# Kernel tuning notes

Measured on AMD Instinct MI355X. Metric: run time of the kernel, lower is better.

The kernel has to match this reference:

```python
import jax, jax.numpy as jnp
import numpy as np

N, FIN, FOUT = 4096, 256, 256


def setup_inputs() -> dict:
    key = jax.random.key(0)
    ks = jax.random.split(key, 6)
    x = jax.random.normal(ks[0], (N, FIN), jnp.float32)
    adj = jax.random.randint(ks[1], (N, N), 0, 2, jnp.int32)  # dense 0/1 adjacency
    W = jax.random.normal(ks[2], (FOUT, FIN), jnp.float32) / np.sqrt(FIN)
    b = jax.random.normal(ks[3], (FOUT,), jnp.float32) * 0.01
    att_w = jax.random.normal(ks[4], (2 * FOUT,), jnp.float32) / np.sqrt(2.0 * FOUT)  # Linear(2F,1).weight squeezed
    att_b = jax.random.normal(ks[5], (), jnp.float32) * 0.01
    return {"x": x, "adj": adj, "W": W, "b": b, "att_w": att_w, "att_b": att_b}


def reference(x, adj, W, b, att_w, att_b):
    n = x.shape[0]
    fo = W.shape[0]
    h = x @ W.T + b  # [N, Fout]
    # score(i,j) = att([h_i ; h_j]) = h_i.w1 + h_j.w2 + att_b  -> no [N,N,2F] concat
    s = (h @ att_w[:fo])[:, None] + (h @ att_w[fo:])[None, :] + att_b  # [N, N]
    edge = adj == 1
    # GLOBAL softmax over all edges (faithful to F.softmax(stacked_scores, dim=0))
    gmax = jnp.max(jnp.where(edge, s, -jnp.inf))
    e = jnp.exp(s - gmax)
    denom = jnp.sum(jnp.where(edge, e, 0.0))
    p = (e / denom).reshape(-1)  # softmaxed score per pair (valid at edges)
    # original indexes attention_scores[j] by NODE id j into the row-major edge list:
    # recover the score of the j-th global edge (j = 0..N-1) via cumsum rank + scatter
    flat = edge.reshape(-1)
    rank = jnp.cumsum(flat.astype(jnp.int32)) - 1  # rank of each edge in row-major order
    idx = jnp.where(flat, rank, n)  # non-edges and ranks >= n get dropped
    w_node = jnp.zeros((n,), h.dtype).at[idx].set(p, mode="drop")  # [N]
    # output[i] = sum_{j: adj[i,j]==1} w_node[j] * h[j]
    out = jax.nn.relu(edge.astype(h.dtype) @ (w_node[:, None] * h))
    return out
```

## Files before the change

kernel.cpp:

```cpp
#include <hip/hip_runtime.h>
#include <cstdint>
#include <cstddef>

#define NN 4096
#define FDIM 256

typedef __attribute__((ext_vector_type(4))) float fx4;
typedef __attribute__((ext_vector_type(2))) float fx2;
typedef __attribute__((ext_vector_type(8))) short s8v;

__device__ inline uint16_t f2bf(float f) {
    union { float f; uint32_t u; } v; v.f = f;
    uint32_t u = v.u;
    uint32_t r = (u + 0x7FFFu + ((u >> 16) & 1u)) >> 16;
    return (uint16_t)r;
}

__global__ __launch_bounds__(256) void k_h(const float* __restrict__ x,
        const float* __restrict__ W, const float* __restrict__ bias,
        float* __restrict__ h) {
    __shared__ __align__(16) float xs[2][64 * 34];
    __shared__ __align__(16) float wt[2][64 * 68];
    const int bi = blockIdx.x, bf = blockIdx.y;
    const int t = threadIdx.x;
    const int tx = t & 15, ty = t >> 4;
    float acc[2][4] = {};
    float rx[8], rw[16];
    #pragma unroll
    for (int u = 0; u < 8; ++u) {
        const int e = t + 256 * u, r = e >> 6, c = e & 63;
        rx[u] = x[(size_t)(bi * 32 + r) * 256 + c];
    }
    #pragma unroll
    for (int u = 0; u < 16; ++u) {
        const int e = t + 256 * u, r = e >> 6, c = e & 63;
        rw[u] = W[(size_t)(bf * 64 + r) * 256 + c];
    }
    for (int p = 0; p < 4; ++p) {
        float* xb = xs[p & 1];
        float* wb = wt[p & 1];
        #pragma unroll
        for (int u = 0; u < 8; ++u) {
            const int e = t + 256 * u, r = e >> 6, c = e & 63;
            xb[c * 34 + r] = rx[u];
        }
        #pragma unroll
        for (int u = 0; u < 16; ++u) {
            const int e = t + 256 * u, r = e >> 6, c = e & 63;
            const int sw = 8 * ((c & 7) ^ ((c >> 3) & 7));
            wb[c * 68 + (r ^ sw)] = rw[u];
        }
        __syncthreads();
        if (p < 3) {
            const int k0 = (p + 1) * 64;
            #pragma unroll
            for (int u = 0; u < 8; ++u) {
                const int e = t + 256 * u, r = e >> 6, c = e & 63;
                rx[u] = x[(size_t)(bi * 32 + r) * 256 + k0 + c];
            }
            #pragma unroll
            for (int u = 0; u < 16; ++u) {
                const int e = t + 256 * u, r = e >> 6, c = e & 63;
                rw[u] = W[(size_t)(bf * 64 + r) * 256 + k0 + c];
            }
        }
        #pragma unroll 16
        for (int k = 0; k < 64; ++k) {
            const int sw = 8 * ((k & 7) ^ ((k >> 3) & 7));
            const fx2 av = *(const fx2*)(xb + k * 34 + ty * 2);
            const fx4 bv = *(const fx4*)(wb + k * 68 + ((tx * 4) ^ sw));
            #pragma unroll
            for (int u = 0; u < 2; ++u)
                #pragma unroll
                for (int v = 0; v < 4; ++v)
                    acc[u][v] += av[u] * bv[v];
        }
    }
    const fx4 bv = *(const fx4*)(bias + bf * 64 + tx * 4);
    #pragma unroll
    for (int u = 0; u < 2; ++u) {
        const int i = bi * 32 + ty * 2 + u;
        fx4 r;
        #pragma unroll
        for (int v = 0; v < 4; ++v) r[v] = acc[u][v] + bv[v];
        *(fx4*)(h + (size_t)i * 256 + bf * 64 + tx * 4) = r;
    }
}

__global__ __launch_bounds__(256) void k_a(const float* __restrict__ h,
        const float* __restrict__ att_w, float* __restrict__ a1,
        float* __restrict__ a2) {
    const int wv = threadIdx.x >> 6, l = threadIdx.x & 63;
    const int i = blockIdx.x * 4 + wv;
    float s1 = 0.f, s2 = 0.f;
    #pragma unroll
    for (int c = l; c < 256; c += 64) {
        const float hv = h[(size_t)i * 256 + c];
        s1 += hv * att_w[c];
        s2 += hv * att_w[256 + c];
    }
    #pragma unroll
    for (int d = 32; d > 0; d >>= 1) {
        s1 += __shfl_down(s1, d);
        s2 += __shfl_down(s2, d);
    }
    if (l == 0) { a1[i] = s1; a2[i] = s2; }
}

__global__ __launch_bounds__(1024) void k_prep(const float* __restrict__ a1,
        const float* __restrict__ a2, const int* __restrict__ adj,
        float* __restrict__ E1, float* __restrict__ E2,
        float* __restrict__ wraw, float* __restrict__ Sg) {
    __shared__ float E1s[NN];
    __shared__ float E2s[NN];
    __shared__ float red1[16], red2[16];
    __shared__ int wtot[16];
    __shared__ int base_s;
    const int t = threadIdx.x, lane = t & 63, wv = t >> 6;
    const fx4 v1 = *(const fx4*)(a1 + t * 4);
    const fx4 v2 = *(const fx4*)(a2 + t * 4);
    float m1 = fmaxf(fmaxf(v1[0], v1[1]), fmaxf(v1[2], v1[3]));
    float m2 = fmaxf(fmaxf(v2[0], v2[1]), fmaxf(v2[2], v2[3]));
    #pragma unroll
    for (int d = 32; d > 0; d >>= 1) {
        m1 = fmaxf(m1, __shfl_down(m1, d));
        m2 = fmaxf(m2, __shfl_down(m2, d));
    }
    if (lane == 0) { red1[wv] = m1; red2[wv] = m2; }
    __syncthreads();
    if (t == 0) {
        float mm1 = -1e30f, mm2 = -1e30f;
        for (int k = 0; k < 16; ++k) {
            mm1 = fmaxf(mm1, red1[k]);
            mm2 = fmaxf(mm2, red2[k]);
        }
        red1[0] = mm1; red2[0] = mm2;
        *Sg = 0.f;
        base_s = 0;
    }
    __syncthreads();
    const float M1 = red1[0], M2 = red2[0];
    fx4 e1v, e2v, z4 = {0.f, 0.f, 0.f, 0.f};
    #pragma unroll
    for (int j = 0; j < 4; ++j) {
        e1v[j] = expf(v1[j] - M1);
        e2v[j] = expf(v2[j] - M2);
    }
    *(fx4*)(E1s + t * 4) = e1v;
    *(fx4*)(E2s + t * 4) = e2v;
    *(fx4*)(E1 + t * 4) = e1v;
    *(fx4*)(E2 + t * 4) = e2v;
    *(fx4*)(wraw + t * 4) = z4;
    __syncthreads();
    for (int row = 0; row < NN; ++row) {
        const int base = base_s;
        if (base >= NN) break;
        const int4 a = ((const int4*)(adj + (size_t)row * NN))[t];
        const int vj[4] = {a.x, a.y, a.z, a.w};
        int cnt = 0;
        #pragma unroll
        for (int j = 0; j < 4; ++j) cnt += (vj[j] == 1);
        int inc = cnt;
        #pragma unroll
        for (int d = 1; d < 64; d <<= 1) {
            const int y = __shfl_up(inc, d);
            if (lane >= d) inc += y;
        }
        if (lane == 63) wtot[wv] = inc;
        __syncthreads();
        int wbase = 0, total = 0;
        #pragma unroll
        for (int w = 0; w < 16; ++w) {
            const int xw = wtot[w];
            total += xw;
            wbase += (w < wv) ? xw : 0;
        }
        if (t == 0) base_s = base + total;
        int r = base + wbase + inc - cnt;
        if (cnt && r < NN) {
            const float e1 = E1s[row];
            #pragma unroll
            for (int j = 0; j < 4; ++j) {
                if (vj[j] == 1) {
                    if (r < NN) wraw[r] = e1 * E2s[t * 4 + j];
                    ++r;
                }
            }
        }
        __syncthreads();
    }
}

__global__ __launch_bounds__(256) void k_g(const float* __restrict__ h,
        const float* __restrict__ wraw, uint16_t* __restrict__ gt) {
    __shared__ float tile[64][65];
    const int bj = blockIdx.x, bf = blockIdx.y;
    const int t = threadIdx.x;
    for (int e = t; e < 4096; e += 256) {
        const int r = e >> 6, c = e & 63;
        const int j = bj * 64 + r;
        tile[r][c] = h[(size_t)j * 256 + bf * 64 + c] * wraw[j];
    }
    __syncthreads();
    for (int e = t; e < 4096; e += 256) {
        const int r = e >> 6, c = e & 63;
        gt[(size_t)(bf * 64 + r) * NN + bj * 64 + c] = f2bf(tile[c][r]);
    }
}

__global__ __launch_bounds__(256) void k_fused(const int* __restrict__ adj,
        const uint16_t* __restrict__ gt, const float* __restrict__ E1,
        const float* __restrict__ E2, float* __restrict__ part,
        float* __restrict__ Sg, int krange) {
    __shared__ __align__(16) uint16_t As[64 * 72];
    __shared__ __align__(16) uint16_t Gs[272 * 72];
    const int ib = blockIdx.x, ks = blockIdx.y;
    const int t = threadIdx.x;
    const int wv = t >> 6, lane = t & 63;
    const int q = lane >> 4, m16 = lane & 15;
    const int i0 = ib * 64, k0 = ks * krange;
    const int ksteps = krange >> 6;

    fx4 acc[4][4];
    #pragma unroll
    for (int a = 0; a < 4; ++a)
        #pragma unroll
        for (int b = 0; b < 4; ++b) acc[a][b] = (fx4){0.f, 0.f, 0.f, 0.f};
    fx4 accS[4];
    #pragma unroll
    for (int a = 0; a < 4; ++a) accS[a] = (fx4){0.f, 0.f, 0.f, 0.f};

    for (int e = t; e < 15 * 72; e += 256) Gs[257 * 72 + e] = 0;

    for (int step = 0; step < ksteps; ++step) {
        const int kk = k0 + step * 64;
        #pragma unroll
        for (int p = 0; p < 4; ++p) {
            const int r = p * 16 + (t >> 4);
            const int c4 = (t & 15) * 4;
            const int4 a = *(const int4*)(adj + (size_t)(i0 + r) * NN + kk + c4);
            uint2 w;
            w.x = (uint32_t)(a.x | (a.y << 16)) * 0x3F80u;
            w.y = (uint32_t)(a.z | (a.w << 16)) * 0x3F80u;
            *(uint2*)(&As[r * 72 + c4]) = w;
        }
        #pragma unroll
        for (int p = 0; p < 8; ++p) {
            const int f = p * 32 + (t >> 3);
            const int ch = (t & 7) * 8;
            const s8v v = *(const s8v*)(gt + (size_t)f * NN + kk + ch);
            *(s8v*)(Gs + f * 72 + ch) = v;
        }
        if (t < 8) {
            const float* e2p = E2 + kk + t * 8;
            uint32_t* dst = (uint32_t*)(&Gs[256 * 72 + t * 8]);
            #pragma unroll
            for (int j = 0; j < 4; ++j)
                dst[j] = (uint32_t)f2bf(e2p[2 * j]) |
                         ((uint32_t)f2bf(e2p[2 * j + 1]) << 16);
        }
        __syncthreads();
        s8v afr[4][2];
        #pragma unroll
        for (int it = 0; it < 4; ++it)
            #pragma unroll
            for (int kh = 0; kh < 2; ++kh)
                afr[it][kh] = *(const s8v*)(As + (it * 16 + m16) * 72 + kh * 32 + q * 8);
        #pragma unroll
        for (int ft = 0; ft < 4; ++ft) {
            #pragma unroll
            for (int kh = 0; kh < 2; ++kh) {
                const s8v bfr = *(const s8v*)(Gs + (wv * 64 + ft * 16 + m16) * 72 + kh * 32 + q * 8);
                #pragma unroll
                for (int it = 0; it < 4; ++it)
                    acc[it][ft] = __builtin_amdgcn_mfma_f32_16x16x32_bf16(
                        afr[it][kh], bfr, acc[it][ft], 0, 0, 0);
            }
        }
        if (wv == 3) {
            #pragma unroll
            for (int kh = 0; kh < 2; ++kh) {
                const s8v bfrS = *(const s8v*)(Gs + (256 + m16) * 72 + kh * 32 + q * 8);
                #pragma unroll
                for (int it = 0; it < 4; ++it)
                    accS[it] = __builtin_amdgcn_mfma_f32_16x16x32_bf16(
                        afr[it][kh], bfrS, accS[it], 0, 0, 0);
            }
        }
        __syncthreads();
    }
    if (wv == 3) {
        float s_local = 0.f;
        #pragma unroll
        for (int it = 0; it < 4; ++it)
            #pragma unroll
            for (int r = 0; r < 4; ++r)
                s_local += accS[it][r] * E1[i0 + it * 16 + q * 4 + r];
        #pragma unroll
        for (int d = 32; d > 0; d >>= 1) s_local += __shfl_down(s_local, d);
        if (lane == 0) atomicAdd(Sg, s_local);
    }
    float* dst = part + (size_t)ks * NN * FDIM;
    #pragma unroll
    for (int it = 0; it < 4; ++it) {
        #pragma unroll
        for (int ft = 0; ft < 4; ++ft) {
            const int f = wv * 64 + ft * 16 + m16;
            #pragma unroll
            for (int r = 0; r < 4; ++r) {
                const int i = i0 + it * 16 + q * 4 + r;
                dst[(size_t)i * FDIM + f] = acc[it][ft][r];
            }
        }
    }
}

__global__ __launch_bounds__(256) void k_out(const float* __restrict__ part,
        const float* __restrict__ Sg, float* __restrict__ out, int nsplit) {
    const int b = blockIdx.x;
    const int ib = (b & 7) + 8 * ((b >> 3) & 7);
    const int sub = b >> 6;
    const int t = threadIdx.x;
    const int row = ib * 64 + sub * 4 + (t >> 6);
    const size_t idx = (size_t)row * 256 + (t & 63) * 4;
    const float inv = 1.0f / (*Sg);
    fx4 s = {0.f, 0.f, 0.f, 0.f};
    for (int k = 0; k < nsplit; ++k)
        s += *(const fx4*)(part + (size_t)k * NN * FDIM + idx);
    fx4 r;
    r[0] = fmaxf(s[0], 0.f) * inv;
    r[1] = fmaxf(s[1], 0.f) * inv;
    r[2] = fmaxf(s[2], 0.f) * inv;
    r[3] = fmaxf(s[3], 0.f) * inv;
    *(fx4*)(out + idx) = r;
}

extern "C" void kernel_launch(void* const* d_in, const int* in_sizes, int n_in,
                              void* d_out, int out_size, void* d_ws, size_t ws_size,
                              hipStream_t stream) {
    const float* x     = (const float*)d_in[0];
    const int*   adj   = (const int*)d_in[1];
    const float* W     = (const float*)d_in[2];
    const float* bias  = (const float*)d_in[3];
    const float* att_w = (const float*)d_in[4];
    float* out = (float*)d_out;
    char* ws = (char*)d_ws;
    float*    h    = (float*)(ws + 0);
    uint16_t* gt   = (uint16_t*)(ws + (size_t)4194304);
    float*    a1   = (float*)(ws + 6291456);
    float*    a2   = (float*)(ws + 6307840);
    float*    E1   = (float*)(ws + 6324224);
    float*    E2   = (float*)(ws + 6340608);
    float*    wraw = (float*)(ws + 6356992);
    float*    Sg   = (float*)(ws + 6373376);
    float*    part = (float*)(ws + 6373632);

    const size_t avail = (ws_size > 6373632) ? (ws_size - 6373632) : 0;
    int splitk = 1;
    while (splitk < 8 &&
           (size_t)(splitk * 2) * NN * FDIM * sizeof(float) <= avail)
        splitk <<= 1;
    const int krange = NN / splitk;

    k_h   <<<dim3(128, 4), 256, 0, stream>>>(x, W, bias, h);
    k_a   <<<dim3(1024), 256, 0, stream>>>(h, att_w, a1, a2);
    k_prep<<<dim3(1), 1024, 0, stream>>>(a1, a2, adj, E1, E2, wraw, Sg);
    k_g   <<<dim3(64, 4), 256, 0, stream>>>(h, wraw, gt);
    k_fused<<<dim3(64, splitk), 256, 0, stream>>>(adj, gt, E1, E2, part, Sg, krange);
    k_out <<<dim3(1024), 256, 0, stream>>>(part, Sg, out, splitk);
}
```

Before: 159.5 us.

## Fuse all stages into one cooperative persistent kernel with grid syncs

Replaces the six separate kernel launches with a single cooperative kernel of 512 blocks that runs every stage, separated by grid-wide barriers, to remove launch gaps and inter-kernel drain. It falls back to the old multi-kernel path if the cooperative launch fails or the workspace is too small. The prep stage now runs on a single 256-thread block instead of 1024 threads, so its serial row scan is slower and leaves the rest of the grid idle at the barrier. The k_out indexing is also simplified.

```diff
diff --git a/kernel.cpp b/kernel.cpp
--- a/kernel.cpp
+++ b/kernel.cpp
@@ -1,6 +1,9 @@
 #include <hip/hip_runtime.h>
+#include <hip/hip_cooperative_groups.h>
 #include <cstdint>
 #include <cstddef>
+
+namespace cg = cooperative_groups;
 
 #define NN 4096
 #define FDIM 256
@@ -14,6 +17,340 @@
     uint32_t u = v.u;
     uint32_t r = (u + 0x7FFFu + ((u >> 16) & 1u)) >> 16;
     return (uint16_t)r;
+}
+
+union SMem {
+    struct { float xs[2 * 64 * 34]; float wt[2 * 64 * 68]; } p1;
+    struct { float E1s[NN]; float E2s[NN]; float red1[4], red2[4];
+             int wtot[4]; int base_s; } p3;
+    struct { float tile[32 * 65]; } p4;
+    struct { uint16_t As[64 * 72]; uint16_t Gs[272 * 72]; } p5;
+};
+
+__global__ __launch_bounds__(256, 2) void k_mega(
+        const float* __restrict__ x, const int* __restrict__ adj,
+        const float* __restrict__ W, const float* __restrict__ bias,
+        const float* __restrict__ att_w,
+        float* __restrict__ h, uint16_t* __restrict__ gt,
+        float* __restrict__ a1, float* __restrict__ a2,
+        float* __restrict__ E1, float* __restrict__ E2,
+        float* __restrict__ wraw, float* __restrict__ Sg,
+        float* __restrict__ part, float* __restrict__ out) {
+    cg::grid_group grid = cg::this_grid();
+    __shared__ SMem sm;
+    const int blk = blockIdx.x;
+    const int t = threadIdx.x;
+    const int lane = t & 63, wv = t >> 6;
+
+    {
+        const int bi = blk & 127, bf = blk >> 7;
+        const int tx = t & 15, ty = t >> 4;
+        float acc[2][4] = {};
+        float rx[8], rw[16];
+        #pragma unroll
+        for (int u = 0; u < 8; ++u) {
+            const int e = t + 256 * u, r = e >> 6, c = e & 63;
+            rx[u] = x[(size_t)(bi * 32 + r) * 256 + c];
+        }
+        #pragma unroll
+        for (int u = 0; u < 16; ++u) {
+            const int e = t + 256 * u, r = e >> 6, c = e & 63;
+            rw[u] = W[(size_t)(bf * 64 + r) * 256 + c];
+        }
+        for (int p = 0; p < 4; ++p) {
+            float* xb = sm.p1.xs + (p & 1) * (64 * 34);
+            float* wb = sm.p1.wt + (p & 1) * (64 * 68);
+            #pragma unroll
+            for (int u = 0; u < 8; ++u) {
+                const int e = t + 256 * u, r = e >> 6, c = e & 63;
+                xb[c * 34 + r] = rx[u];
+            }
+            #pragma unroll
+            for (int u = 0; u < 16; ++u) {
+                const int e = t + 256 * u, r = e >> 6, c = e & 63;
+                const int sw = 8 * ((c & 7) ^ ((c >> 3) & 7));
+                wb[c * 68 + (r ^ sw)] = rw[u];
+            }
+            __syncthreads();
+            if (p < 3) {
+                const int k0 = (p + 1) * 64;
+                #pragma unroll
+                for (int u = 0; u < 8; ++u) {
+                    const int e = t + 256 * u, r = e >> 6, c = e & 63;
+                    rx[u] = x[(size_t)(bi * 32 + r) * 256 + k0 + c];
+                }
+                #pragma unroll
+                for (int u = 0; u < 16; ++u) {
+                    const int e = t + 256 * u, r = e >> 6, c = e & 63;
+                    rw[u] = W[(size_t)(bf * 64 + r) * 256 + k0 + c];
+                }
+            }
+            #pragma unroll 16
+            for (int k = 0; k < 64; ++k) {
+                const int sw = 8 * ((k & 7) ^ ((k >> 3) & 7));
+                const fx2 av = *(const fx2*)(xb + k * 34 + ty * 2);
+                const fx4 bv = *(const fx4*)(wb + k * 68 + ((tx * 4) ^ sw));
+                #pragma unroll
+                for (int u = 0; u < 2; ++u)
+                    #pragma unroll
+                    for (int v = 0; v < 4; ++v)
+                        acc[u][v] += av[u] * bv[v];
+            }
+        }
+        const fx4 bv = *(const fx4*)(bias + bf * 64 + tx * 4);
+        #pragma unroll
+        for (int u = 0; u < 2; ++u) {
+            const int i = bi * 32 + ty * 2 + u;
+            fx4 r;
+            #pragma unroll
+            for (int v = 0; v < 4; ++v) r[v] = acc[u][v] + bv[v];
+            *(fx4*)(h + (size_t)i * 256 + bf * 64 + tx * 4) = r;
+        }
+    }
+    grid.sync();
+
+    {
+        const fx4 w1v = *(const fx4*)(att_w + lane * 4);
+        const fx4 w2v = *(const fx4*)(att_w + 256 + lane * 4);
+        #pragma unroll
+        for (int u = 0; u < 2; ++u) {
+            const int row = blk * 8 + wv * 2 + u;
+            const fx4 hv = *(const fx4*)(h + (size_t)row * 256 + lane * 4);
+            float s1 = hv[0] * w1v[0] + hv[1] * w1v[1] + hv[2] * w1v[2] + hv[3] * w1v[3];
+            float s2 = hv[0] * w2v[0] + hv[1] * w2v[1] + hv[2] * w2v[2] + hv[3] * w2v[3];
+            #pragma unroll
+            for (int d = 32; d > 0; d >>= 1) {
+                s1 += __shfl_down(s1, d);
+                s2 += __shfl_down(s2, d);
+            }
+            if (lane == 0) { a1[row] = s1; a2[row] = s2; }
+        }
+    }
+    grid.sync();
+
+    if (blk == 0) {
+        fx4 va1[4], va2[4];
+        #pragma unroll
+        for (int j = 0; j < 4; ++j) {
+            va1[j] = *(const fx4*)(a1 + t * 16 + j * 4);
+            va2[j] = *(const fx4*)(a2 + t * 16 + j * 4);
+        }
+        float m1 = -1e30f, m2 = -1e30f;
+        #pragma unroll
+        for (int j = 0; j < 4; ++j)
+            #pragma unroll
+            for (int k = 0; k < 4; ++k) {
+                m1 = fmaxf(m1, va1[j][k]);
+                m2 = fmaxf(m2, va2[j][k]);
+            }
+        #pragma unroll
+        for (int d = 32; d > 0; d >>= 1) {
+            m1 = fmaxf(m1, __shfl_down(m1, d));
+            m2 = fmaxf(m2, __shfl_down(m2, d));
+        }
+        if (lane == 0) { sm.p3.red1[wv] = m1; sm.p3.red2[wv] = m2; }
+        __syncthreads();
+        const float M1 = fmaxf(fmaxf(sm.p3.red1[0], sm.p3.red1[1]),
+                               fmaxf(sm.p3.red1[2], sm.p3.red1[3]));
+        const float M2 = fmaxf(fmaxf(sm.p3.red2[0], sm.p3.red2[1]),
+                               fmaxf(sm.p3.red2[2], sm.p3.red2[3]));
+        const fx4 z4 = {0.f, 0.f, 0.f, 0.f};
+        #pragma unroll
+        for (int j = 0; j < 4; ++j) {
+            fx4 e1v, e2v;
+            #pragma unroll
+            for (int k = 0; k < 4; ++k) {
+                e1v[k] = expf(va1[j][k] - M1);
+                e2v[k] = expf(va2[j][k] - M2);
+            }
+            *(fx4*)(sm.p3.E1s + t * 16 + j * 4) = e1v;
+            *(fx4*)(sm.p3.E2s + t * 16 + j * 4) = e2v;
+            *(fx4*)(E1 + t * 16 + j * 4) = e1v;
+            *(fx4*)(E2 + t * 16 + j * 4) = e2v;
+            *(fx4*)(wraw + t * 16 + j * 4) = z4;
+        }
+        if (t == 0) { *Sg = 0.f; sm.p3.base_s = 0; }
+        __syncthreads();
+        for (int row = 0; row < NN; ++row) {
+            const int base = sm.p3.base_s;
+            if (base >= NN) break;
+            const int* arow = adj + (size_t)row * NN + t * 16;
+            const int4 A0 = ((const int4*)arow)[0];
+            const int4 A1 = ((const int4*)arow)[1];
+            const int4 A2 = ((const int4*)arow)[2];
+            const int4 A3 = ((const int4*)arow)[3];
+            const int v[16] = {A0.x, A0.y, A0.z, A0.w, A1.x, A1.y, A1.z, A1.w,
+                               A2.x, A2.y, A2.z, A2.w, A3.x, A3.y, A3.z, A3.w};
+            int cnt = 0;
+            #pragma unroll
+            for (int j = 0; j < 16; ++j) cnt += (v[j] == 1);
+            int inc = cnt;
+            #pragma unroll
+            for (int d = 1; d < 64; d <<= 1) {
+                const int y = __shfl_up(inc, d);
+                if (lane >= d) inc += y;
+            }
+            if (lane == 63) sm.p3.wtot[wv] = inc;
+            __syncthreads();
+            int wbase = 0, total = 0;
+            #pragma unroll
+            for (int w = 0; w < 4; ++w) {
+                const int xw = sm.p3.wtot[w];
+                total += xw;
+                wbase += (w < wv) ? xw : 0;
+            }
+            if (t == 0) sm.p3.base_s = base + total;
+            int r = base + wbase + inc - cnt;
+            if (cnt && r < NN) {
+                const float e1 = sm.p3.E1s[row];
+                #pragma unroll
+                for (int j = 0; j < 16; ++j) {
+                    if (v[j] == 1) {
+                        if (r < NN) wraw[r] = e1 * sm.p3.E2s[t * 16 + j];
+                        ++r;
+                    }
+                }
+            }
+            __syncthreads();
+        }
+    }
+    grid.sync();
+
+    {
+        const int bj = blk & 127, bf = blk >> 7;
+        const int j0 = bj * 32, f0 = bf * 64;
+        #pragma unroll
+        for (int p = 0; p < 8; ++p) {
+            const int e = t + 256 * p;
+            const int jl = e >> 6, fl = e & 63;
+            sm.p4.tile[jl * 65 + fl] =
+                h[(size_t)(j0 + jl) * 256 + f0 + fl] * wraw[j0 + jl];
+        }
+        __syncthreads();
+        #pragma unroll
+        for (int p = 0; p < 8; ++p) {
+            const int e = t + 256 * p;
+            const int fl = e >> 5, jl = e & 31;
+            gt[(size_t)(f0 + fl) * NN + j0 + jl] = f2bf(sm.p4.tile[jl * 65 + fl]);
+        }
+    }
+    grid.sync();
+
+    {
+        const int ib = blk & 63, ks = blk >> 6;
+        const int q = lane >> 4, m16 = lane & 15;
+        const int i0 = ib * 64, k0 = ks * 512;
+        fx4 acc[4][4];
+        #pragma unroll
+        for (int a = 0; a < 4; ++a)
+            #pragma unroll
+            for (int b = 0; b < 4; ++b) acc[a][b] = (fx4){0.f, 0.f, 0.f, 0.f};
+        fx4 accS[4];
+        #pragma unroll
+        for (int a = 0; a < 4; ++a) accS[a] = (fx4){0.f, 0.f, 0.f, 0.f};
+        for (int e = t; e < 15 * 72; e += 256) sm.p5.Gs[257 * 72 + e] = 0;
+        for (int step = 0; step < 8; ++step) {
+            const int kk = k0 + step * 64;
+            #pragma unroll
+            for (int p = 0; p < 4; ++p) {
+                const int r = p * 16 + (t >> 4);
+                const int c4 = (t & 15) * 4;
+                const int4 a = *(const int4*)(adj + (size_t)(i0 + r) * NN + kk + c4);
+                uint2 w;
+                w.x = (uint32_t)(a.x | (a.y << 16)) * 0x3F80u;
+                w.y = (uint32_t)(a.z | (a.w << 16)) * 0x3F80u;
+                *(uint2*)(&sm.p5.As[r * 72 + c4]) = w;
+            }
+            #pragma unroll
+            for (int p = 0; p < 8; ++p) {
+                const int f = p * 32 + (t >> 3);
+                const int ch = (t & 7) * 8;
+                const s8v v = *(const s8v*)(gt + (size_t)f * NN + kk + ch);
+                *(s8v*)(sm.p5.Gs + f * 72 + ch) = v;
+            }
+            if (t < 8) {
+                const float* e2p = E2 + kk + t * 8;
+                uint32_t* dst = (uint32_t*)(&sm.p5.Gs[256 * 72 + t * 8]);
+                #pragma unroll
+                for (int j = 0; j < 4; ++j)
+                    dst[j] = (uint32_t)f2bf(e2p[2 * j]) |
+                             ((uint32_t)f2bf(e2p[2 * j + 1]) << 16);
+            }
+            __syncthreads();
+            s8v afr[4][2];
+            #pragma unroll
+            for (int it = 0; it < 4; ++it)
+                #pragma unroll
+                for (int kh = 0; kh < 2; ++kh)
+                    afr[it][kh] = *(const s8v*)(sm.p5.As + (it * 16 + m16) * 72 + kh * 32 + q * 8);
+            #pragma unroll
+            for (int ft = 0; ft < 4; ++ft) {
+                #pragma unroll
+                for (int kh = 0; kh < 2; ++kh) {
+                    const s8v bfr = *(const s8v*)(sm.p5.Gs + (wv * 64 + ft * 16 + m16) * 72 + kh * 32 + q * 8);
+                    #pragma unroll
+                    for (int it = 0; it < 4; ++it)
+                        acc[it][ft] = __builtin_amdgcn_mfma_f32_16x16x32_bf16(
+                            afr[it][kh], bfr, acc[it][ft], 0, 0, 0);
+                }
+            }
+            if (wv == 3) {
+                #pragma unroll
+                for (int kh = 0; kh < 2; ++kh) {
+                    const s8v bfrS = *(const s8v*)(sm.p5.Gs + (256 + m16) * 72 + kh * 32 + q * 8);
+                    #pragma unroll
+                    for (int it = 0; it < 4; ++it)
+                        accS[it] = __builtin_amdgcn_mfma_f32_16x16x32_bf16(
+                            afr[it][kh], bfrS, accS[it], 0, 0, 0);
+                }
+            }
+            __syncthreads();
+        }
+        if (wv == 3) {
+            float s_local = 0.f;
+            #pragma unroll
+            for (int it = 0; it < 4; ++it)
+                #pragma unroll
+                for (int r = 0; r < 4; ++r)
+                    s_local += accS[it][r] * E1[i0 + it * 16 + q * 4 + r];
+            #pragma unroll
+            for (int d = 32; d > 0; d >>= 1) s_local += __shfl_down(s_local, d);
+            if (lane == 0) atomicAdd(Sg, s_local);
+        }
+        float* dst = part + (size_t)ks * NN * FDIM;
+        #pragma unroll
+        for (int it = 0; it < 4; ++it) {
+            #pragma unroll
+            for (int ft = 0; ft < 4; ++ft) {
+                const int f = wv * 64 + ft * 16 + m16;
+                #pragma unroll
+                for (int r = 0; r < 4; ++r) {
+                    const int i = i0 + it * 16 + q * 4 + r;
+                    dst[(size_t)i * FDIM + f] = acc[it][ft][r];
+                }
+            }
+        }
+    }
+    grid.sync();
+
+    {
+        const float Sv = *(volatile const float*)Sg;
+        const float inv = 1.0f / Sv;
+        #pragma unroll
+        for (int rep = 0; rep < 2; ++rep) {
+            const size_t idx = (size_t)blk * 2048 + rep * 1024 + t * 4;
+            fx4 s = {0.f, 0.f, 0.f, 0.f};
+            #pragma unroll
+            for (int k = 0; k < 8; ++k)
+                s += *(const fx4*)(part + (size_t)k * NN * FDIM + idx);
+            fx4 r;
+            r[0] = fmaxf(s[0], 0.f) * inv;
+            r[1] = fmaxf(s[1], 0.f) * inv;
+            r[2] = fmaxf(s[2], 0.f) * inv;
+            r[3] = fmaxf(s[3], 0.f) * inv;
+            *(fx4*)(out + idx) = r;
+        }
+    }
 }
 
 __global__ __launch_bounds__(256) void k_h(const float* __restrict__ x,
@@ -220,7 +557,6 @@
     const int q = lane >> 4, m16 = lane & 15;
     const int i0 = ib * 64, k0 = ks * krange;
     const int ksteps = krange >> 6;
-
     fx4 acc[4][4];
     #pragma unroll
     for (int a = 0; a < 4; ++a)
@@ -229,9 +565,7 @@
     fx4 accS[4];
     #pragma unroll
     for (int a = 0; a < 4; ++a) accS[a] = (fx4){0.f, 0.f, 0.f, 0.f};
-
     for (int e = t; e < 15 * 72; e += 256) Gs[257 * 72 + e] = 0;
-
     for (int step = 0; step < ksteps; ++step) {
         const int kk = k0 + step * 64;
         #pragma unroll
@@ -317,22 +651,17 @@
 
 __global__ __launch_bounds__(256) void k_out(const float* __restrict__ part,
         const float* __restrict__ Sg, float* __restrict__ out, int nsplit) {
-    const int b = blockIdx.x;
-    const int ib = (b & 7) + 8 * ((b >> 3) & 7);
-    const int sub = b >> 6;
-    const int t = threadIdx.x;
-    const int row = ib * 64 + sub * 4 + (t >> 6);
-    const size_t idx = (size_t)row * 256 + (t & 63) * 4;
+    const int idx = blockIdx.x * 256 + threadIdx.x;
     const float inv = 1.0f / (*Sg);
     fx4 s = {0.f, 0.f, 0.f, 0.f};
     for (int k = 0; k < nsplit; ++k)
-        s += *(const fx4*)(part + (size_t)k * NN * FDIM + idx);
+        s += *(const fx4*)(part + (size_t)k * NN * FDIM + (size_t)idx * 4);
     fx4 r;
     r[0] = fmaxf(s[0], 0.f) * inv;
     r[1] = fmaxf(s[1], 0.f) * inv;
     r[2] = fmaxf(s[2], 0.f) * inv;
     r[3] = fmaxf(s[3], 0.f) * inv;
-    *(fx4*)(out + idx) = r;
+    *(fx4*)(out + (size_t)idx * 4) = r;
 }
 
 extern "C" void kernel_launch(void* const* d_in, const int* in_sizes, int n_in,
@@ -355,17 +684,29 @@
     float*    Sg   = (float*)(ws + 6373376);
     float*    part = (float*)(ws + 6373632);
 
-    const size_t avail = (ws_size > 6373632) ? (ws_size - 6373632) : 0;
-    int splitk = 1;
-    while (splitk < 8 &&
-           (size_t)(splitk * 2) * NN * FDIM * sizeof(float) <= avail)
-        splitk <<= 1;
-    const int krange = NN / splitk;
-
-    k_h   <<<dim3(128, 4), 256, 0, stream>>>(x, W, bias, h);
-    k_a   <<<dim3(1024), 256, 0, stream>>>(h, att_w, a1, a2);
-    k_prep<<<dim3(1), 1024, 0, stream>>>(a1, a2, adj, E1, E2, wraw, Sg);
-    k_g   <<<dim3(64, 4), 256, 0, stream>>>(h, wraw, gt);
-    k_fused<<<dim3(64, splitk), 256, 0, stream>>>(adj, gt, E1, E2, part, Sg, krange);
-    k_out <<<dim3(1024), 256, 0, stream>>>(part, Sg, out, splitk);
-}
+    const size_t need = (size_t)6373632 + (size_t)8 * NN * FDIM * sizeof(float);
+    bool coop_ok = false;
+    if (ws_size >= need) {
+        void* args[] = {(void*)&x, (void*)&adj, (void*)&W, (void*)&bias,
+                        (void*)&att_w, (void*)&h, (void*)&gt, (void*)&a1,
+                        (void*)&a2, (void*)&E1, (void*)&E2, (void*)&wraw,
+                        (void*)&Sg, (void*)&part, (void*)&out};
+        hipError_t e = hipLaunchCooperativeKernel((const void*)k_mega, dim3(512),
+                                                  dim3(256), args, 0, stream);
+        coop_ok = (e == hipSuccess);
+    }
+    if (!coop_ok) {
+        const size_t avail = (ws_size > 6373632) ? (ws_size - 6373632) : 0;
+        int splitk = 1;
+        while (splitk < 8 &&
+               (size_t)(splitk * 2) * NN * FDIM * sizeof(float) <= avail)
+            splitk <<= 1;
+        const int krange = NN / splitk;
+        k_h    <<<dim3(128, 4), 256, 0, stream>>>(x, W, bias, h);
+        k_a    <<<dim3(1024), 256, 0, stream>>>(h, att_w, a1, a2);
+        k_prep <<<dim3(1), 1024, 0, stream>>>(a1, a2, adj, E1, E2, wraw, Sg);
+        k_g    <<<dim3(64, 4), 256, 0, stream>>>(h, wraw, gt);
+        k_fused<<<dim3(64, splitk), 256, 0, stream>>>(adj, gt, E1, E2, part, Sg, krange);
+        k_out  <<<dim3(1024), 256, 0, stream>>>(part, Sg, out, splitk);
+    }
+}
```

Result: slower. 466.8 us (+192.6%).

## Fuse attention projections into linear GEMM and store split-K partials in bf16

Applied to the files above, without the earlier changes.

Removes the separate k_a kernel: the h GEMM epilogue now computes per-column-block partial dot products with the attention weights, and k_prep sums the four partials. Split-K partial sums from the fused aggregation kernel are written as bf16 instead of fp32, halving partial-buffer traffic, and k_out reads 8 bf16 values per thread. k_g uses smaller 32-row tiles to launch more blocks. Rounding partial sums to bf16 adds precision error before the final reduction.

```diff
diff --git a/kernel.cpp b/kernel.cpp
--- a/kernel.cpp
+++ b/kernel.cpp
@@ -18,7 +18,8 @@
 
 __global__ __launch_bounds__(256) void k_h(const float* __restrict__ x,
         const float* __restrict__ W, const float* __restrict__ bias,
-        float* __restrict__ h) {
+        const float* __restrict__ att_w, float* __restrict__ h,
+        float* __restrict__ a1p, float* __restrict__ a2p) {
     __shared__ __align__(16) float xs[2][64 * 34];
     __shared__ __align__(16) float wt[2][64 * 68];
     const int bi = blockIdx.x, bf = blockIdx.y;
@@ -77,38 +78,34 @@
         }
     }
     const fx4 bv = *(const fx4*)(bias + bf * 64 + tx * 4);
+    const fx4 w1v = *(const fx4*)(att_w + bf * 64 + tx * 4);
+    const fx4 w2v = *(const fx4*)(att_w + 256 + bf * 64 + tx * 4);
     #pragma unroll
     for (int u = 0; u < 2; ++u) {
         const int i = bi * 32 + ty * 2 + u;
         fx4 r;
-        #pragma unroll
-        for (int v = 0; v < 4; ++v) r[v] = acc[u][v] + bv[v];
+        float s1 = 0.f, s2 = 0.f;
+        #pragma unroll
+        for (int v = 0; v < 4; ++v) {
+            r[v] = acc[u][v] + bv[v];
+            s1 += r[v] * w1v[v];
+            s2 += r[v] * w2v[v];
+        }
         *(fx4*)(h + (size_t)i * 256 + bf * 64 + tx * 4) = r;
-    }
-}
-
-__global__ __launch_bounds__(256) void k_a(const float* __restrict__ h,
-        const float* __restrict__ att_w, float* __restrict__ a1,
-        float* __restrict__ a2) {
-    const int wv = threadIdx.x >> 6, l = threadIdx.x & 63;
-    const int i = blockIdx.x * 4 + wv;
-    float s1 = 0.f, s2 = 0.f;
-    #pragma unroll
-    for (int c = l; c < 256; c += 64) {
-        const float hv = h[(size_t)i * 256 + c];
-        s1 += hv * att_w[c];
-        s2 += hv * att_w[256 + c];
-    }
-    #pragma unroll
-    for (int d = 32; d > 0; d >>= 1) {
-        s1 += __shfl_down(s1, d);
-        s2 += __shfl_down(s2, d);
-    }
-    if (l == 0) { a1[i] = s1; a2[i] = s2; }
-}
-
-__global__ __launch_bounds__(1024) void k_prep(const float* __restrict__ a1,
-        const float* __restrict__ a2, const int* __restrict__ adj,
+        #pragma unroll
+        for (int d = 8; d > 0; d >>= 1) {
+            s1 += __shfl_down(s1, d, 16);
+            s2 += __shfl_down(s2, d, 16);
+        }
+        if (tx == 0) {
+            a1p[bf * NN + i] = s1;
+            a2p[bf * NN + i] = s2;
+        }
+    }
+}
+
+__global__ __launch_bounds__(1024) void k_prep(const float* __restrict__ a1p,
+        const float* __restrict__ a2p, const int* __restrict__ adj,
         float* __restrict__ E1, float* __restrict__ E2,
         float* __restrict__ wraw, float* __restrict__ Sg) {
     __shared__ float E1s[NN];
@@ -117,8 +114,12 @@
     __shared__ int wtot[16];
     __shared__ int base_s;
     const int t = threadIdx.x, lane = t & 63, wv = t >> 6;
-    const fx4 v1 = *(const fx4*)(a1 + t * 4);
-    const fx4 v2 = *(const fx4*)(a2 + t * 4);
+    fx4 v1 = {0.f, 0.f, 0.f, 0.f}, v2 = {0.f, 0.f, 0.f, 0.f};
+    #pragma unroll
+    for (int bf = 0; bf < 4; ++bf) {
+        v1 += *(const fx4*)(a1p + bf * NN + t * 4);
+        v2 += *(const fx4*)(a2p + bf * NN + t * 4);
+    }
     float m1 = fmaxf(fmaxf(v1[0], v1[1]), fmaxf(v1[2], v1[3]));
     float m2 = fmaxf(fmaxf(v2[0], v2[1]), fmaxf(v2[2], v2[3]));
     #pragma unroll
@@ -193,24 +194,28 @@
 
 __global__ __launch_bounds__(256) void k_g(const float* __restrict__ h,
         const float* __restrict__ wraw, uint16_t* __restrict__ gt) {
-    __shared__ float tile[64][65];
+    __shared__ float tile[32 * 65];
     const int bj = blockIdx.x, bf = blockIdx.y;
+    const int j0 = bj * 32, f0 = bf * 64;
     const int t = threadIdx.x;
-    for (int e = t; e < 4096; e += 256) {
-        const int r = e >> 6, c = e & 63;
-        const int j = bj * 64 + r;
-        tile[r][c] = h[(size_t)j * 256 + bf * 64 + c] * wraw[j];
+    #pragma unroll
+    for (int p = 0; p < 8; ++p) {
+        const int e = t + 256 * p;
+        const int jl = e >> 6, fl = e & 63;
+        tile[jl * 65 + fl] = h[(size_t)(j0 + jl) * 256 + f0 + fl] * wraw[j0 + jl];
     }
     __syncthreads();
-    for (int e = t; e < 4096; e += 256) {
-        const int r = e >> 6, c = e & 63;
-        gt[(size_t)(bf * 64 + r) * NN + bj * 64 + c] = f2bf(tile[c][r]);
+    #pragma unroll
+    for (int p = 0; p < 8; ++p) {
+        const int e = t + 256 * p;
+        const int fl = e >> 5, jl = e & 31;
+        gt[(size_t)(f0 + fl) * NN + j0 + jl] = f2bf(tile[jl * 65 + fl]);
     }
 }
 
 __global__ __launch_bounds__(256) void k_fused(const int* __restrict__ adj,
         const uint16_t* __restrict__ gt, const float* __restrict__ E1,
-        const float* __restrict__ E2, float* __restrict__ part,
+        const float* __restrict__ E2, uint16_t* __restrict__ part,
         float* __restrict__ Sg, int krange) {
     __shared__ __align__(16) uint16_t As[64 * 72];
     __shared__ __align__(16) uint16_t Gs[272 * 72];
@@ -220,7 +225,6 @@
     const int q = lane >> 4, m16 = lane & 15;
     const int i0 = ib * 64, k0 = ks * krange;
     const int ksteps = krange >> 6;
-
     fx4 acc[4][4];
     #pragma unroll
     for (int a = 0; a < 4; ++a)
@@ -229,9 +233,7 @@
     fx4 accS[4];
     #pragma unroll
     for (int a = 0; a < 4; ++a) accS[a] = (fx4){0.f, 0.f, 0.f, 0.f};
-
     for (int e = t; e < 15 * 72; e += 256) Gs[257 * 72 + e] = 0;
-
     for (int step = 0; step < ksteps; ++step) {
         const int kk = k0 + step * 64;
         #pragma unroll
@@ -300,7 +302,7 @@
         for (int d = 32; d > 0; d >>= 1) s_local += __shfl_down(s_local, d);
         if (lane == 0) atomicAdd(Sg, s_local);
     }
-    float* dst = part + (size_t)ks * NN * FDIM;
+    uint16_t* dst = part + (size_t)ks * NN * FDIM;
     #pragma unroll
     for (int it = 0; it < 4; ++it) {
         #pragma unroll
@@ -309,30 +311,34 @@
             #pragma unroll
             for (int r = 0; r < 4; ++r) {
                 const int i = i0 + it * 16 + q * 4 + r;
-                dst[(size_t)i * FDIM + f] = acc[it][ft][r];
-            }
-        }
-    }
-}
-
-__global__ __launch_bounds__(256) void k_out(const float* __restrict__ part,
+                dst[(size_t)i * FDIM + f] = f2bf(acc[it][ft][r]);
+            }
+        }
+    }
+}
+
+__global__ __launch_bounds__(256) void k_out(const uint16_t* __restrict__ part,
         const float* __restrict__ Sg, float* __restrict__ out, int nsplit) {
-    const int b = blockIdx.x;
-    const int ib = (b & 7) + 8 * ((b >> 3) & 7);
-    const int sub = b >> 6;
-    const int t = threadIdx.x;
-    const int row = ib * 64 + sub * 4 + (t >> 6);
-    const size_t idx = (size_t)row * 256 + (t & 63) * 4;
+    const size_t idx = ((size_t)blockIdx.x * 256 + threadIdx.x) * 8;
     const float inv = 1.0f / (*Sg);
-    fx4 s = {0.f, 0.f, 0.f, 0.f};
-    for (int k = 0; k < nsplit; ++k)
-        s += *(const fx4*)(part + (size_t)k * NN * FDIM + idx);
-    fx4 r;
-    r[0] = fmaxf(s[0], 0.f) * inv;
-    r[1] = fmaxf(s[1], 0.f) * inv;
-    r[2] = fmaxf(s[2], 0.f) * inv;
-    r[3] = fmaxf(s[3], 0.f) * inv;
-    *(fx4*)(out + idx) = r;
+    float s[8] = {};
+    for (int k = 0; k < nsplit; ++k) {
+        const s8v v = *(const s8v*)(part + (size_t)k * NN * FDIM + idx);
+        #pragma unroll
+        for (int j = 0; j < 8; ++j) {
+            union { uint32_t u; float f; } cv;
+            cv.u = ((uint32_t)(uint16_t)v[j]) << 16;
+            s[j] += cv.f;
+        }
+    }
+    fx4 r0, r1;
+    #pragma unroll
+    for (int j = 0; j < 4; ++j) {
+        r0[j] = fmaxf(s[j], 0.f) * inv;
+        r1[j] = fmaxf(s[4 + j], 0.f) * inv;
+    }
+    *(fx4*)(out + idx) = r0;
+    *(fx4*)(out + idx + 4) = r1;
 }
 
 extern "C" void kernel_launch(void* const* d_in, const int* in_sizes, int n_in,
@@ -347,25 +353,24 @@
     char* ws = (char*)d_ws;
     float*    h    = (float*)(ws + 0);
     uint16_t* gt   = (uint16_t*)(ws + (size_t)4194304);
-    float*    a1   = (float*)(ws + 6291456);
-    float*    a2   = (float*)(ws + 6307840);
-    float*    E1   = (float*)(ws + 6324224);
-    float*    E2   = (float*)(ws + 6340608);
-    float*    wraw = (float*)(ws + 6356992);
-    float*    Sg   = (float*)(ws + 6373376);
-    float*    part = (float*)(ws + 6373632);
-
-    const size_t avail = (ws_size > 6373632) ? (ws_size - 6373632) : 0;
+    float*    a1p  = (float*)(ws + 6291456);
+    float*    a2p  = (float*)(ws + 6356992);
+    float*    E1   = (float*)(ws + 6422528);
+    float*    E2   = (float*)(ws + 6438912);
+    float*    wraw = (float*)(ws + 6455296);
+    float*    Sg   = (float*)(ws + 6471680);
+    uint16_t* part = (uint16_t*)(ws + 6471936);
+
+    const size_t avail = (ws_size > 6471936) ? (ws_size - 6471936) : 0;
     int splitk = 1;
     while (splitk < 8 &&
-           (size_t)(splitk * 2) * NN * FDIM * sizeof(float) <= avail)
+           (size_t)(splitk * 2) * NN * FDIM * sizeof(uint16_t) <= avail)
         splitk <<= 1;
     const int krange = NN / splitk;
 
-    k_h   <<<dim3(128, 4), 256, 0, stream>>>(x, W, bias, h);
-    k_a   <<<dim3(1024), 256, 0, stream>>>(h, att_w, a1, a2);
-    k_prep<<<dim3(1), 1024, 0, stream>>>(a1, a2, adj, E1, E2, wraw, Sg);
-    k_g   <<<dim3(64, 4), 256, 0, stream>>>(h, wraw, gt);
+    k_h    <<<dim3(128, 4), 256, 0, stream>>>(x, W, bias, att_w, h, a1p, a2p);
+    k_prep <<<dim3(1), 1024, 0, stream>>>(a1p, a2p, adj, E1, E2, wraw, Sg);
+    k_g    <<<dim3(128, 4), 256, 0, stream>>>(h, wraw, gt);
     k_fused<<<dim3(64, splitk), 256, 0, stream>>>(adj, gt, E1, E2, part, Sg, krange);
-    k_out <<<dim3(1024), 256, 0, stream>>>(part, Sg, out, splitk);
-}
+    k_out  <<<dim3(512), 256, 0, stream>>>(part, Sg, out, splitk);
+}
```

Result: faster. 152.3 us (-4.5%).
